# Optimization experiments

Measured on AMD Instinct MI355X. Metric: run time of the kernel, lower is better.

Reference implementation:

```python
import jax, jax.numpy as jnp
import numpy as np
import math

N, C, V, T = 64, 192, 25, 300
D = 192  # dim2

def setup_inputs() -> dict:
    key = jax.random.key(0)
    k0, k1, k2, k3 = jax.random.split(key, 4)
    x1 = jax.random.normal(k0, (N, C, V, T), dtype=jnp.float32)
    w1 = jax.random.normal(k1, (D, C), dtype=jnp.float32) * 0.05
    w2 = jax.random.normal(k2, (D, C), dtype=jnp.float32) * 0.05
    w_mask = jax.random.normal(k3, (1, C), dtype=jnp.float32) * 0.05
    return {"x1": x1, "w1": w1, "w2": w2, "w_mask": w_mask}

def reference(x1, w1, w2, w_mask):
    # 1x1 conv projections: contract over channel dim C -> D, layout [N,T,D,V]
    g1 = jnp.einsum('ncvt,dc->ntdv', x1, w1)
    g2 = jnp.einsum('ncvt,dc->ntdv', x1, w2)
    # mean-center over the joint axis V (matches g.mean(2) on [B, D, V])
    g1 = g1 - g1.mean(axis=-1, keepdims=True)
    g2 = g2 - g2.mean(axis=-1, keepdims=True)
    scale = math.sqrt(D)
    # sim_map[n,t,v,w] = sum_d g1[n,t,d,v] * g2[n,t,d,w]
    sim = jnp.einsum('ntdv,ntdw->ntvw', g1, g2) / scale
    # mask: 1x1 conv to 1 channel -> [N,T,V], broadcast over rows (added along last dim)
    mask = jnp.einsum('ncvt,c->ntv', x1, w_mask[0])  # [N,T,V]
    logits = sim + mask[:, :, None, :]
    out = jax.nn.softmax(logits, axis=-1)  # [N, T, V, V]
    return out
```

## Files before the change

### kernel.cpp

```cpp
#include <hip/hip_runtime.h>
#include <hip/hip_bf16.h>
#include <cstdint>
#include <cstddef>

#define NN 64
#define CC 192
#define VV 25
#define TTT 300
#define TC 16
#define NTC 19
#define GRID (NN*NTC)

#define MFRAG_OFF 40960
#define WML_OFF 77824

#define RAW_STRIDE 13312
#define TILE_OFF 26624
#define TILE_STRIDE 6512
#define YS_OFF 39648
#define MLDS_OFF 88800
#define WMLDS_OFF 162528
#define LDS_TOTAL 162912
#define MCPY_CHUNKS 4632

typedef unsigned short u16;
typedef unsigned long long u64;
typedef short bf16x8 __attribute__((ext_vector_type(8)));
typedef float f32x4 __attribute__((ext_vector_type(4)));
typedef float f4 __attribute__((ext_vector_type(4)));
typedef int i32x4 __attribute__((ext_vector_type(4)));

__device__ __forceinline__ u16 f2bf(float x) {
  union { float f; uint32_t u; } v; v.f = x;
  uint32_t r = v.u + 0x7fffu + ((v.u >> 16) & 1u);
  return (u16)(r >> 16);
}
__device__ __forceinline__ u64 pack4(f32x4 a) {
  return (u64)f2bf(a[0]) | ((u64)f2bf(a[1]) << 16) |
         ((u64)f2bf(a[2]) << 32) | ((u64)f2bf(a[3]) << 48);
}

__global__ __launch_bounds__(192) void prep(const float* __restrict__ w1,
                                            const float* __restrict__ w2,
                                            const float* __restrict__ wm,
                                            u16* __restrict__ mb) {
  int c2 = threadIdx.x, b = blockIdx.x;
  if (b < CC) {
    float s = 0.f;
    for (int d = 0; d < CC; ++d) s += w1[d * CC + b] * w2[d * CC + c2];
    u16 h = f2bf(s);
    int cc = b >> 5, half = (b >> 4) & 1, lr = b & 15;
    int ks = c2 >> 5, l8 = (c2 & 31) >> 3, e = c2 & 7;
    int lane = l8 * 16 + lr;
    mb[MFRAG_OFF + (((cc * 2 + half) * 6 + ks) * 64 + lane) * 8 + e] = h;
  } else {
    mb[WML_OFF + c2] = f2bf(wm[c2]);
  }
}

__global__ __launch_bounds__(1024, 4) void fused(const float* __restrict__ x1,
                                                 const u16* __restrict__ mb,
                                                 float* __restrict__ out) {
  extern __shared__ char lds[];
  const int tid = threadIdx.x;
  const int wid = tid >> 6, lane = tid & 63, lr = lane & 15, lq = lane >> 4;
  char* YS = lds + YS_OFF + wid * 3072;

  int b = blockIdx.x;
  int logical = (b & 7) * (GRID / 8) + (b >> 3);
  int n = logical / NTC;
  int ch = logical - n * NTC;
  int t0 = ch * TC;
  int t = t0 + wid;
  const bool lastch = (t0 + TC > TTT);

  const float* xb = x1 + (size_t)n * (CC * VV * TTT) + t0;

  auto issueDMA = [&](int ct) {
    if (wid < 13) {
      int k = wid * 64 + lane;
      int kk = k > 799 ? 799 : k;
      int cl = kk / 100;
      int rem = kk - cl * 100;
      int v = rem >> 2;
      int seg = kk & 3;
      int sege = (lastch && seg == 3) ? 2 : seg;
      const float* src = xb + (size_t)(ct * 8 + cl) * (VV * TTT) + v * TTT + sege * 4;
      char* dst = lds + (ct & 1) * RAW_STRIDE + wid * 1024;
      __builtin_amdgcn_global_load_lds(
          (const __attribute__((address_space(1))) void*)src,
          (__attribute__((address_space(3))) void*)dst, 16, 0, 0);
    }
  };

  asm volatile("s_waitcnt vmcnt(0)" ::: "memory");
  issueDMA(0);

  {
    const char* src = (const char*)mb + (size_t)MFRAG_OFF * 2;
    #pragma unroll
    for (int k = 0; k < 5; ++k) {
      int i = k * 1024 + tid;
      if (i < MCPY_CHUNKS)
        *(i32x4*)(lds + MLDS_OFF + i * 16) = *(const i32x4*)(src + i * 16);
    }
  }

  bf16x8 sf[2][6];
  for (int ct = 0; ct < 24; ++ct) {
    __builtin_amdgcn_s_barrier();
    if (ct < 23) {
      issueDMA(ct + 1);
      asm volatile("s_waitcnt vmcnt(1)" ::: "memory");
    } else {
      asm volatile("s_waitcnt vmcnt(0)" ::: "memory");
    }
    __builtin_amdgcn_s_barrier();

    if (tid < 800) {
      int cl = tid / 100;
      int rem = tid - cl * 100;
      int v = rem >> 2;
      int seg = tid & 3;
      f4 a = *(const f4*)(lds + (ct & 1) * RAW_STRIDE + tid * 16);
      char* tb = lds + TILE_OFF + (ct & 1) * TILE_STRIDE + (size_t)v * 16 + cl * 2;
      *(u16*)(tb + (size_t)(seg * 4 + 0) * 25 * 16) = f2bf(a[0]);
      *(u16*)(tb + (size_t)(seg * 4 + 1) * 25 * 16) = f2bf(a[1]);
      *(u16*)(tb + (size_t)(seg * 4 + 2) * 25 * 16) = f2bf(a[2]);
      *(u16*)(tb + (size_t)(seg * 4 + 3) * 25 * 16) = f2bf(a[3]);
    }

    if (ct > 0) {
      const int cp = ct - 1;
      if (lq == (cp & 3)) {
        const char* tp = lds + TILE_OFF + (cp & 1) * TILE_STRIDE;
        sf[0][cp >> 2] = *(const bf16x8*)(tp + (size_t)(wid * VV + lr) * 16);
        sf[1][cp >> 2] = *(const bf16x8*)(tp + (size_t)(wid * VV + 16 + lr) * 16);
      }
    }
  }
  __syncthreads();
  {
    const int cp = 23;
    if (lq == (cp & 3)) {
      const char* tp = lds + TILE_OFF + (cp & 1) * TILE_STRIDE;
      sf[0][cp >> 2] = *(const bf16x8*)(tp + (size_t)(wid * VV + lr) * 16);
      sf[1][cp >> 2] = *(const bf16x8*)(tp + (size_t)(wid * VV + 16 + lr) * 16);
    }
  }

  f32x4 pacc[2][2], macc[2];
  #pragma unroll
  for (int i = 0; i < 2; ++i) {
    macc[i] = (f32x4){0.f, 0.f, 0.f, 0.f};
    #pragma unroll
    for (int jx = 0; jx < 2; ++jx) pacc[i][jx] = (f32x4){0.f, 0.f, 0.f, 0.f};
  }
  const char* mfl = lds + MLDS_OFF;

  __builtin_amdgcn_s_setprio(1);
  #pragma unroll
  for (int cc = 0; cc < 6; ++cc) {
    f32x4 y00 = (f32x4){0.f,0.f,0.f,0.f}, y01 = y00, y10 = y00, y11 = y00;
    #pragma unroll
    for (int ks = 0; ks < 6; ++ks) {
      bf16x8 a0 = *(const bf16x8*)(mfl + (size_t)((cc * 12 + ks) * 64 + lane) * 16);
      bf16x8 a1 = *(const bf16x8*)(mfl + (size_t)((cc * 12 + 6 + ks) * 64 + lane) * 16);
      y00 = __builtin_amdgcn_mfma_f32_16x16x32_bf16(a0, sf[0][ks], y00, 0, 0, 0);
      y01 = __builtin_amdgcn_mfma_f32_16x16x32_bf16(a1, sf[0][ks], y01, 0, 0, 0);
      y10 = __builtin_amdgcn_mfma_f32_16x16x32_bf16(a0, sf[1][ks], y10, 0, 0, 0);
      y11 = __builtin_amdgcn_mfma_f32_16x16x32_bf16(a1, sf[1][ks], y11, 0, 0, 0);
    }
    *(u64*)(YS + (lr) * 80 + lq * 8) = pack4(y00);
    *(u64*)(YS + (lr) * 80 + 32 + lq * 8) = pack4(y01);
    *(u64*)(YS + (16 + lr) * 80 + lq * 8) = pack4(y10);
    *(u64*)(YS + (16 + lr) * 80 + 32 + lq * 8) = pack4(y11);

    bf16x8 wmf = *(const bf16x8*)(lds + WMLDS_OFF + (cc * 32 + lq * 8) * 2);
    macc[0] = __builtin_amdgcn_mfma_f32_16x16x32_bf16(sf[0][cc], wmf, macc[0], 0, 0, 0);
    macc[1] = __builtin_amdgcn_mfma_f32_16x16x32_bf16(sf[1][cc], wmf, macc[1], 0, 0, 0);

    bf16x8 B0 = *(const bf16x8*)(YS + (lr) * 80 + lq * 16);
    bf16x8 B1 = *(const bf16x8*)(YS + (16 + lr) * 80 + lq * 16);
    pacc[0][0] = __builtin_amdgcn_mfma_f32_16x16x32_bf16(sf[0][cc], B0, pacc[0][0], 0, 0, 0);
    pacc[0][1] = __builtin_amdgcn_mfma_f32_16x16x32_bf16(sf[0][cc], B1, pacc[0][1], 0, 0, 0);
    pacc[1][0] = __builtin_amdgcn_mfma_f32_16x16x32_bf16(sf[1][cc], B0, pacc[1][0], 0, 0, 0);
    pacc[1][1] = __builtin_amdgcn_mfma_f32_16x16x32_bf16(sf[1][cc], B1, pacc[1][1], 0, 0, 0);
  }
  __builtin_amdgcn_s_setprio(0);

  float* SIMW = (float*)YS;
  #pragma unroll
  for (int vt = 0; vt < 2; ++vt)
    #pragma unroll
    for (int wt = 0; wt < 2; ++wt) {
      int w = wt * 16 + lr;
      if (w < VV) {
        #pragma unroll
        for (int i = 0; i < 4; ++i) {
          int v = vt * 16 + lq * 4 + i;
          if (v < VV) SIMW[v * 28 + w] = pacc[vt][wt][i];
        }
      }
    }
  if (lr == 0) {
    #pragma unroll
    for (int j = 0; j < 2; ++j)
      #pragma unroll
      for (int i = 0; i < 4; ++i) {
        int v = j * 16 + lq * 4 + i;
        if (v < VV) SIMW[26 * 28 + v] = macc[j][i];
      }
  }

  f32x4 r[6];
  float r24 = 0.f, rs = 0.f, cs = 0.f;
  if (lane < VV) {
    const f32x4* rp = (const f32x4*)(SIMW + lane * 28);
    #pragma unroll
    for (int k = 0; k < 6; ++k) r[k] = rp[k];
    r24 = SIMW[lane * 28 + 24];
    f32x4 s4 = r[0] + r[1] + r[2] + r[3] + r[4] + r[5];
    rs = s4[0] + s4[1] + s4[2] + s4[3] + r24;
    #pragma unroll
    for (int v = 0; v < VV; ++v) cs += SIMW[v * 28 + lane];
    SIMW[25 * 28 + lane] = cs;
  }
  float x = (lane < VV) ? cs : 0.f;
  #pragma unroll
  for (int s = 1; s < 64; s <<= 1) x += __shfl_xor(x, s);
  const float tot = x;

  if (lane < VV) {
    const int v = lane;
    const float base = -rs * 0.04f + tot * 0.0016f;
    const float isc = 0.07216878364870323f;
    const f32x4* cp4 = (const f32x4*)(SIMW + 25 * 28);
    const f32x4* mp = (const f32x4*)(SIMW + 26 * 28);
    float l[VV];
    float mx = -1e30f;
    #pragma unroll
    for (int k = 0; k < 6; ++k) {
      f32x4 val = (r[k] - cp4[k] * 0.04f + base) * isc + mp[k];
      #pragma unroll
      for (int j = 0; j < 4; ++j) {
        l[k * 4 + j] = val[j];
        mx = fmaxf(mx, val[j]);
      }
    }
    {
      float val = (r24 - SIMW[25 * 28 + 24] * 0.04f + base) * isc + SIMW[26 * 28 + 24];
      l[24] = val;
      mx = fmaxf(mx, val);
    }
    float sum = 0.f;
    #pragma unroll
    for (int w = 0; w < VV; ++w) { float e = __expf(l[w] - mx); l[w] = e; sum += e; }
    float rsc = 1.0f / sum;
    f32x4* wp = (f32x4*)(SIMW + v * 28);
    #pragma unroll
    for (int k = 0; k < 6; ++k) {
      f32x4 o = (f32x4){l[k*4] * rsc, l[k*4+1] * rsc, l[k*4+2] * rsc, l[k*4+3] * rsc};
      wp[k] = o;
    }
    SIMW[v * 28 + 24] = l[24] * rsc;
  }

  if (t < TTT) {
    float* ob = out + (size_t)(n * TTT + t) * 625;
    int v = (lane * 1311) >> 15;
    int w = lane - v * 25;
    #pragma unroll
    for (int i = 0; i < 10; ++i) {
      int idx = lane + i * 64;
      if (idx < 625) ob[idx] = SIMW[v * 28 + w];
      w += 14; v += 2;
      if (w >= 25) { w -= 25; ++v; }
    }
  }
}

extern "C" void kernel_launch(void* const* d_in, const int* in_sizes, int n_in,
                              void* d_out, int out_size, void* d_ws, size_t ws_size,
                              hipStream_t stream) {
  const float* x1 = (const float*)d_in[0];
  const float* w1 = (const float*)d_in[1];
  const float* w2 = (const float*)d_in[2];
  const float* wm = (const float*)d_in[3];
  float* out = (float*)d_out;
  u16* mb = (u16*)d_ws;

  hipLaunchKernelGGL(prep, dim3(CC + 1), dim3(CC), 0, stream, w1, w2, wm, mb);
  hipLaunchKernelGGL(fused, dim3(GRID), dim3(1024), LDS_TOTAL, stream, x1, mb, out);
}
```

Before: 167.7 us.

## Halve time chunk per block and read M fragments from global instead of LDS

Each block now covers 8 time steps with 512 threads instead of 16 with 1024, which doubles the grid and shrinks the LDS staging buffers. The 147 KB LDS copy of the bf16 M-matrix fragments is removed, and the MFMA A-operands and mask weights are loaded straight from global/L2 memory. Dropping LDS from about 160 KB to about 45 KB per block should let several blocks share a CU, hiding latency. In exchange, every wave now fetches the M fragments from global memory inside the MFMA loop, and the wave priority boost is removed.

Measured after the change: 195.9 us. +16.9%, slower.

```diff
diff --git a/kernel.cpp b/kernel.cpp
--- a/kernel.cpp
+++ b/kernel.cpp
@@ -7,28 +7,24 @@
 #define CC 192
 #define VV 25
 #define TTT 300
-#define TC 16
-#define NTC 19
+#define TC 8
+#define NTC 38
 #define GRID (NN*NTC)
 
 #define MFRAG_OFF 40960
 #define WML_OFF 77824
 
-#define RAW_STRIDE 13312
-#define TILE_OFF 26624
-#define TILE_STRIDE 6512
-#define YS_OFF 39648
-#define MLDS_OFF 88800
-#define WMLDS_OFF 162528
-#define LDS_TOTAL 162912
-#define MCPY_CHUNKS 4632
+#define RAW_STRIDE 7168
+#define TILE_OFF 14336
+#define TILE_STRIDE 3312
+#define YS_OFF 20960
+#define LDS_TOTAL 45536
 
 typedef unsigned short u16;
 typedef unsigned long long u64;
 typedef short bf16x8 __attribute__((ext_vector_type(8)));
 typedef float f32x4 __attribute__((ext_vector_type(4)));
 typedef float f4 __attribute__((ext_vector_type(4)));
-typedef int i32x4 __attribute__((ext_vector_type(4)));
 
 __device__ __forceinline__ u16 f2bf(float x) {
   union { float f; uint32_t u; } v; v.f = x;
@@ -58,10 +54,10 @@
   }
 }
 
-__global__ __launch_bounds__(1024, 4) void fused(const float* __restrict__ x1,
-                                                 const u16* __restrict__ mb,
-                                                 float* __restrict__ out) {
-  extern __shared__ char lds[];
+__global__ __launch_bounds__(512, 4) void fused(const float* __restrict__ x1,
+                                                const u16* __restrict__ mb,
+                                                float* __restrict__ out) {
+  __shared__ char lds[LDS_TOTAL];
   const int tid = threadIdx.x;
   const int wid = tid >> 6, lane = tid & 63, lr = lane & 15, lq = lane >> 4;
   char* YS = lds + YS_OFF + wid * 3072;
@@ -77,14 +73,14 @@
   const float* xb = x1 + (size_t)n * (CC * VV * TTT) + t0;
 
   auto issueDMA = [&](int ct) {
-    if (wid < 13) {
+    if (wid < 7) {
       int k = wid * 64 + lane;
-      int kk = k > 799 ? 799 : k;
-      int cl = kk / 100;
-      int rem = kk - cl * 100;
-      int v = rem >> 2;
-      int seg = kk & 3;
-      int sege = (lastch && seg == 3) ? 2 : seg;
+      int kk = k > 399 ? 399 : k;
+      int cl = kk / 50;
+      int rem = kk - cl * 50;
+      int v = rem >> 1;
+      int seg = kk & 1;
+      int sege = (lastch && seg == 1) ? 0 : seg;
       const float* src = xb + (size_t)(ct * 8 + cl) * (VV * TTT) + v * TTT + sege * 4;
       char* dst = lds + (ct & 1) * RAW_STRIDE + wid * 1024;
       __builtin_amdgcn_global_load_lds(
@@ -95,16 +91,6 @@
 
   asm volatile("s_waitcnt vmcnt(0)" ::: "memory");
   issueDMA(0);
-
-  {
-    const char* src = (const char*)mb + (size_t)MFRAG_OFF * 2;
-    #pragma unroll
-    for (int k = 0; k < 5; ++k) {
-      int i = k * 1024 + tid;
-      if (i < MCPY_CHUNKS)
-        *(i32x4*)(lds + MLDS_OFF + i * 16) = *(const i32x4*)(src + i * 16);
-    }
-  }
 
   bf16x8 sf[2][6];
   for (int ct = 0; ct < 24; ++ct) {
@@ -117,17 +103,17 @@
     }
     __builtin_amdgcn_s_barrier();
 
-    if (tid < 800) {
-      int cl = tid / 100;
-      int rem = tid - cl * 100;
-      int v = rem >> 2;
-      int seg = tid & 3;
+    if (tid < 400) {
+      int cl = tid / 50;
+      int rem = tid - cl * 50;
+      int v = rem >> 1;
+      int seg = tid & 1;
       f4 a = *(const f4*)(lds + (ct & 1) * RAW_STRIDE + tid * 16);
       char* tb = lds + TILE_OFF + (ct & 1) * TILE_STRIDE + (size_t)v * 16 + cl * 2;
-      *(u16*)(tb + (size_t)(seg * 4 + 0) * 25 * 16) = f2bf(a[0]);
-      *(u16*)(tb + (size_t)(seg * 4 + 1) * 25 * 16) = f2bf(a[1]);
-      *(u16*)(tb + (size_t)(seg * 4 + 2) * 25 * 16) = f2bf(a[2]);
-      *(u16*)(tb + (size_t)(seg * 4 + 3) * 25 * 16) = f2bf(a[3]);
+      *(u16*)(tb + (size_t)(seg * 4 + 0) * 400) = f2bf(a[0]);
+      *(u16*)(tb + (size_t)(seg * 4 + 1) * 400) = f2bf(a[1]);
+      *(u16*)(tb + (size_t)(seg * 4 + 2) * 400) = f2bf(a[2]);
+      *(u16*)(tb + (size_t)(seg * 4 + 3) * 400) = f2bf(a[3]);
     }
 
     if (ct > 0) {
@@ -156,16 +142,15 @@
     #pragma unroll
     for (int jx = 0; jx < 2; ++jx) pacc[i][jx] = (f32x4){0.f, 0.f, 0.f, 0.f};
   }
-  const char* mfl = lds + MLDS_OFF;
-
-  __builtin_amdgcn_s_setprio(1);
+  const u16* mf = mb + MFRAG_OFF;
+
   #pragma unroll
   for (int cc = 0; cc < 6; ++cc) {
     f32x4 y00 = (f32x4){0.f,0.f,0.f,0.f}, y01 = y00, y10 = y00, y11 = y00;
     #pragma unroll
     for (int ks = 0; ks < 6; ++ks) {
-      bf16x8 a0 = *(const bf16x8*)(mfl + (size_t)((cc * 12 + ks) * 64 + lane) * 16);
-      bf16x8 a1 = *(const bf16x8*)(mfl + (size_t)((cc * 12 + 6 + ks) * 64 + lane) * 16);
+      bf16x8 a0 = *(const bf16x8*)(mf + ((cc * 12 + ks) * 64 + lane) * 8);
+      bf16x8 a1 = *(const bf16x8*)(mf + ((cc * 12 + 6 + ks) * 64 + lane) * 8);
       y00 = __builtin_amdgcn_mfma_f32_16x16x32_bf16(a0, sf[0][ks], y00, 0, 0, 0);
       y01 = __builtin_amdgcn_mfma_f32_16x16x32_bf16(a1, sf[0][ks], y01, 0, 0, 0);
       y10 = __builtin_amdgcn_mfma_f32_16x16x32_bf16(a0, sf[1][ks], y10, 0, 0, 0);
@@ -176,7 +161,7 @@
     *(u64*)(YS + (16 + lr) * 80 + lq * 8) = pack4(y10);
     *(u64*)(YS + (16 + lr) * 80 + 32 + lq * 8) = pack4(y11);
 
-    bf16x8 wmf = *(const bf16x8*)(lds + WMLDS_OFF + (cc * 32 + lq * 8) * 2);
+    bf16x8 wmf = *(const bf16x8*)(mb + WML_OFF + cc * 32 + lq * 8);
     macc[0] = __builtin_amdgcn_mfma_f32_16x16x32_bf16(sf[0][cc], wmf, macc[0], 0, 0, 0);
     macc[1] = __builtin_amdgcn_mfma_f32_16x16x32_bf16(sf[1][cc], wmf, macc[1], 0, 0, 0);
 
@@ -187,7 +172,6 @@
     pacc[1][0] = __builtin_amdgcn_mfma_f32_16x16x32_bf16(sf[1][cc], B0, pacc[1][0], 0, 0, 0);
     pacc[1][1] = __builtin_amdgcn_mfma_f32_16x16x32_bf16(sf[1][cc], B1, pacc[1][1], 0, 0, 0);
   }
-  __builtin_amdgcn_s_setprio(0);
 
   float* SIMW = (float*)YS;
   #pragma unroll
@@ -291,5 +275,5 @@
   u16* mb = (u16*)d_ws;
 
   hipLaunchKernelGGL(prep, dim3(CC + 1), dim3(CC), 0, stream, w1, w2, wm, mb);
-  hipLaunchKernelGGL(fused, dim3(GRID), dim3(1024), LDS_TOTAL, stream, x1, mb, out);
-}
+  hipLaunchKernelGGL(fused, dim3(GRID), dim3(512), 0, stream, x1, mb, out);
+}
```
